# Optimization experiments

Hardware: AMD Instinct MI355X
Metric: run time of the kernel (lower is better)

## Reference

```python
import jax, jax.numpy as jnp
import numpy as np

N, E, G = 50000, 800000, 2000          # nodes, edges, graphs
F_NODE, F_EDGE, H = 64, 16, 128
SLOPE = 0.01                            # leaky_relu slope used throughout AttentiveFP
NUM_ATOM_LAYERS = 2                     # num_layers=3 -> 1 GATEConv + 2 GATConv
NUM_TIMESTEPS = 3


def _leaky(v):
    return jnp.where(v >= 0, v, SLOPE * v)


def _seg_softmax(logits, seg, n):
    # PyG softmax over edges grouped by target segment
    m = jax.ops.segment_max(logits, seg, num_segments=n)
    e = jnp.exp(logits - m[seg])
    s = jax.ops.segment_sum(e, seg, num_segments=n)
    return e / (s[seg] + 1e-16)


def _gru(xi, h, Wih, Whh, bih, bhh):
    # torch.nn.GRUCell, gate order (r, z, n)
    gi = xi @ Wih.T + bih
    gh = h @ Whh.T + bhh
    ir, iz, inn = jnp.split(gi, 3, axis=-1)
    hr, hz, hn = jnp.split(gh, 3, axis=-1)
    r = jax.nn.sigmoid(ir + hr)
    z = jax.nn.sigmoid(iz + hz)
    ng = jnp.tanh(inn + r * hn)
    return (1.0 - z) * ng + z * h


def setup_inputs() -> dict:
    key = jax.random.key(0)
    ks = iter(jax.random.split(key, 64))
    def rn(shape, s=0.1):
        return jax.random.normal(next(ks), shape, jnp.float32) * s
    inp = {}
    inp["x"] = jax.random.normal(next(ks), (N, F_NODE), jnp.float32)
    inp["edge_index"] = jax.random.randint(next(ks), (2, E), 0, N)
    inp["edge_attr"] = jax.random.normal(next(ks), (E, F_EDGE), jnp.float32)
    inp["batch"] = jnp.sort(jax.random.randint(next(ks), (N,), 0, G))
    inp["lin1_W"] = rn((H, F_NODE)); inp["lin1_b"] = rn((H,))
    inp["gate_att_l"] = rn((H,)); inp["gate_att_r"] = rn((H,))
    inp["gate_lin1_W"] = rn((H, H + F_EDGE)); inp["gate_lin2_W"] = rn((H, H)); inp["gate_bias"] = rn((H,))
    inp["gru0_Wih"] = rn((3 * H, H)); inp["gru0_Whh"] = rn((3 * H, H))
    inp["gru0_bih"] = rn((3 * H,)); inp["gru0_bhh"] = rn((3 * H,))
    L = NUM_ATOM_LAYERS
    inp["atom_lin_W"] = rn((L, H, H)); inp["atom_att_src"] = rn((L, H))
    inp["atom_att_dst"] = rn((L, H)); inp["atom_bias"] = rn((L, H))
    inp["atom_gru_Wih"] = rn((L, 3 * H, H)); inp["atom_gru_Whh"] = rn((L, 3 * H, H))
    inp["atom_gru_bih"] = rn((L, 3 * H)); inp["atom_gru_bhh"] = rn((L, 3 * H))
    inp["mol_lin_W"] = rn((H, H)); inp["mol_att_src"] = rn((H,))
    inp["mol_att_dst"] = rn((H,)); inp["mol_bias"] = rn((H,))
    inp["mol_gru_Wih"] = rn((3 * H, H)); inp["mol_gru_Whh"] = rn((3 * H, H))
    inp["mol_gru_bih"] = rn((3 * H,)); inp["mol_gru_bhh"] = rn((3 * H,))
    inp["lin2_W"] = rn((H, H)); inp["lin2_b"] = rn((H,))
    inp["fin_W"] = rn((1, H)); inp["fin_b"] = rn((1,))
    return inp


def _forward(x, edge_attr, lin1_W, lin1_b, gate_att_l, gate_att_r, gate_lin1_W,
             gate_lin2_W, gate_bias, gru0_Wih, gru0_Whh, gru0_bih, gru0_bhh,
             atom_lin_W, atom_att_src, atom_att_dst, atom_bias,
             atom_gru_Wih, atom_gru_Whh, atom_gru_bih, atom_gru_bhh,
             mol_lin_W, mol_att_src, mol_att_dst, mol_bias,
             mol_gru_Wih, mol_gru_Whh, mol_gru_bih, mol_gru_bhh,
             lin2_W, lin2_b, fin_W, fin_b, edge_index, batch):
    src, dst = edge_index[0], edge_index[1]  # PyG: row=source j, col=target i
    # --- input projection ---
    x = _leaky(x @ lin1_W.T + lin1_b)                                     # [N,H]
    # --- GATEConv (edge-featured attention, add aggregation) ---
    hj = _leaky(jnp.concatenate([x[src], edge_attr], axis=-1) @ gate_lin1_W.T)  # [E,H]
    alpha = _leaky(hj @ gate_att_l + (x @ gate_att_r)[dst])               # [E]
    a = _seg_softmax(alpha, dst, N)
    h = jax.ops.segment_sum((x @ gate_lin2_W.T)[src] * a[:, None], dst, num_segments=N) + gate_bias
    h = jax.nn.elu(h)  # dropout is identity in eval mode
    x = jnp.maximum(_gru(h, x, gru0_Wih, gru0_Whh, gru0_bih, gru0_bhh), 0.0)
    # --- atom-level GATConv layers (single head, no self loops) ---
    for l in range(NUM_ATOM_LAYERS):
        xs = x @ atom_lin_W[l].T                                          # [N,H]
        a = _leaky((xs @ atom_att_src[l])[src] + (xs @ atom_att_dst[l])[dst])
        a = _seg_softmax(a, dst, N)
        h = jax.ops.segment_sum(xs[src] * a[:, None], dst, num_segments=N) + atom_bias[l]
        h = jax.nn.elu(h)
        x = jnp.maximum(_gru(h, x, atom_gru_Wih[l], atom_gru_Whh[l],
                             atom_gru_bih[l], atom_gru_bhh[l]), 0.0)
    # --- molecule-level readout: bipartite GATConv node->graph + GRU ---
    out = jnp.maximum(jax.ops.segment_sum(x, batch, num_segments=G), 0.0)  # [G,H]
    xs = x @ mol_lin_W.T                                                   # fixed sources
    a_src = xs @ mol_att_src                                               # [N]
    for _ in range(NUM_TIMESTEPS):
        od = out @ mol_lin_W.T                                             # [G,H]
        a = _leaky(a_src + (od @ mol_att_dst)[batch])
        a = _seg_softmax(a, batch, G)
        h = jax.ops.segment_sum(xs * a[:, None], batch, num_segments=G) + mol_bias
        h = jax.nn.elu(h)
        out = jnp.maximum(_gru(h, out, mol_gru_Wih, mol_gru_Whh, mol_gru_bih, mol_gru_bhh), 0.0)
    out = out @ lin2_W.T + lin2_b                                          # AttentiveFP.lin2
    return jax.nn.sigmoid(out @ fin_W.T + fin_b).squeeze(-1)               # [G]


def reference(x, edge_index, edge_attr, batch, lin1_W, lin1_b, gate_att_l, gate_att_r,
              gate_lin1_W, gate_lin2_W, gate_bias, gru0_Wih, gru0_Whh, gru0_bih, gru0_bhh,
              atom_lin_W, atom_att_src, atom_att_dst, atom_bias,
              atom_gru_Wih, atom_gru_Whh, atom_gru_bih, atom_gru_bhh,
              mol_lin_W, mol_att_src, mol_att_dst, mol_bias,
              mol_gru_Wih, mol_gru_Whh, mol_gru_bih, mol_gru_bhh,
              lin2_W, lin2_b, fin_W, fin_b):
    return _forward(x, edge_attr, lin1_W, lin1_b, gate_att_l, gate_att_r, gate_lin1_W,
                    gate_lin2_W, gate_bias, gru0_Wih, gru0_Whh, gru0_bih, gru0_bhh,
                    atom_lin_W, atom_att_src, atom_att_dst, atom_bias,
                    atom_gru_Wih, atom_gru_Whh, atom_gru_bih, atom_gru_bhh,
                    mol_lin_W, mol_att_src, mol_att_dst, mol_bias,
                    mol_gru_Wih, mol_gru_Whh, mol_gru_bih, mol_gru_bhh,
                    lin2_W, lin2_b, fin_W, fin_b, edge_index, batch)
```

## Files before the change

### kernel.cpp

```cpp
#include <hip/hip_runtime.h>
#include <math.h>

#define NN 50000
#define EE 800000
#define GG 2000
#define HH 128
#define FN 64
#define FE 16

typedef short bf16x8 __attribute__((ext_vector_type(8)));
typedef float f32x4  __attribute__((ext_vector_type(4)));

__device__ __forceinline__ float leakyf(float v){ return v>=0.f ? v : 0.01f*v; }
__device__ __forceinline__ float eluf(float v){ return v>0.f ? v : expm1f(v); }
__device__ __forceinline__ float sigmf(float v){ return 1.f/(1.f+__expf(-v)); }
__device__ __forceinline__ float tanh_fast(float x){
  float ax = fabsf(x);
  float e = __expf(-2.f*ax);
  float t = (1.f - e)/(1.f + e);
  return x>=0.f ? t : -t;
}
__device__ __forceinline__ int rdl(int v, int l){ return __builtin_amdgcn_readlane(v, l); }
__device__ __forceinline__ float rdlf(float v, int l){
  return __int_as_float(__builtin_amdgcn_readlane(__float_as_int(v), l));
}
__device__ __forceinline__ float wsum(float v){
#pragma unroll
  for(int m=32;m>=1;m>>=1) v += __shfl_xor(v,m,64);
  return v;
}
__device__ __forceinline__ float wsum16(float v){
#pragma unroll
  for(int m=8;m>=1;m>>=1) v += __shfl_xor(v,m,64);
  return v;
}
__device__ __forceinline__ float wmax64(float v){
#pragma unroll
  for(int m=32;m>=1;m>>=1) v = fmaxf(v,__shfl_xor(v,m,64));
  return v;
}

__device__ __forceinline__ f32x4 mfma16(bf16x8 a, bf16x8 b, f32x4 c){
  return __builtin_amdgcn_mfma_f32_16x16x32_bf16(a, b, c, 0, 0, 0);
}

__device__ __forceinline__ void splitbf8(const float* p, bf16x8 &hi, bf16x8 &lo){
  float4 u = *(const float4*)p;
  float4 v = *(const float4*)(p+4);
  float f[8] = {u.x,u.y,u.z,u.w,v.x,v.y,v.z,v.w};
#pragma unroll
  for(int i=0;i<8;i++){
    unsigned b = __float_as_uint(f[i]);
    unsigned ht = b & 0xFFFF0000u;
    hi[i] = (short)(b >> 16);
    float r = f[i] - __uint_as_float(ht);
    lo[i] = (short)(__float_as_uint(r) >> 16);
  }
}

#define CV_LIN1   0
#define CV_G1X    8192
#define CV_G2     24576
#define CV_ALIN   40960
#define CV_MOL    73728
#define CV_G0IH   90112
#define CV_G0HH   139264
#define CV_AIH    188416
#define CV_AHH    286720
#define CV_MIH    385024
#define CV_MHH    434176
#define CV_GE     483328
#define CV_TOT2   485376

__global__ void k_convw2(const float* __restrict__ lin1W, const float* __restrict__ glin1W,
                         const float* __restrict__ glin2W, const float* __restrict__ aLinW,
                         const float* __restrict__ aGWih, const float* __restrict__ aGWhh,
                         const float* __restrict__ mLinW, const float* __restrict__ mGWih,
                         const float* __restrict__ mGWhh, const float* __restrict__ g0Wih,
                         const float* __restrict__ g0Whh,
                         short* __restrict__ hi, short* __restrict__ lo){
  int i = blockIdx.x*256 + threadIdx.x;
  if(i >= CV_TOT2) return;
  float v;
  if(i < CV_G1X){            v = lin1W[i];
  } else if(i < CV_G2){      int idx = i - CV_G1X; v = glin1W[(size_t)(idx>>7)*144 + (idx&127)];
  } else if(i < CV_ALIN){    v = glin2W[i - CV_G2];
  } else if(i < CV_MOL){     v = aLinW[i - CV_ALIN];
  } else if(i < CV_G0IH){    v = mLinW[i - CV_MOL];
  } else if(i < CV_G0HH){    v = g0Wih[i - CV_G0IH];
  } else if(i < CV_AIH){     v = g0Whh[i - CV_G0HH];
  } else if(i < CV_AHH){     v = aGWih[i - CV_AIH];
  } else if(i < CV_MIH){     v = aGWhh[i - CV_AHH];
  } else if(i < CV_MHH){     v = mGWih[i - CV_MIH];
  } else if(i < CV_GE){      v = mGWhh[i - CV_MHH];
  } else {                   int idx = i - CV_GE; v = glin1W[(size_t)(idx>>4)*144 + 128 + (idx&15)];
  }
  unsigned b = __float_as_uint(v);
  unsigned ht = b & 0xFFFF0000u;
  hi[i] = (short)(b >> 16);
  float r = v - __uint_as_float(ht);
  lo[i] = (short)(__float_as_uint(r) >> 16);
}

__global__ void k_count_all(const int* __restrict__ esrc, const int* __restrict__ edst,
                            const int* __restrict__ batch,
                            int* __restrict__ degd, int* __restrict__ degs,
                            int* __restrict__ gcnt){
  int i = blockIdx.x*256 + threadIdx.x;
  if(i < EE){
    atomicAdd(&degd[edst[i]], 1);
    atomicAdd(&degs[esrc[i]], 1);
  }
  if(i < NN) atomicAdd(&gcnt[batch[i]], 1);
}

__global__ void k_scan3(const int* __restrict__ degd, const int* __restrict__ degs,
                        const int* __restrict__ gcnt,
                        int* __restrict__ eoff, int* __restrict__ soff, int* __restrict__ goff){
  __shared__ int part[1024];
  const int* cnt; int* off; int n;
  if(blockIdx.x == 0){ cnt = degd; off = eoff; n = NN; }
  else if(blockIdx.x == 1){ cnt = degs; off = soff; n = NN; }
  else { cnt = gcnt; off = goff; n = GG; }
  int t = threadIdx.x;
  int C = (n + 1023) >> 10;
  int lo = t*C, hic = min(lo + C, n);
  int s = 0;
  for(int i=lo;i<hic;i++) s += cnt[i];
  part[t] = s;
  __syncthreads();
  for(int o=1;o<1024;o<<=1){
    int v = (t>=o) ? part[t-o] : 0;
    __syncthreads();
    part[t] += v;
    __syncthreads();
  }
  int base = part[t] - s;
  int run = base;
  for(int i=lo;i<hic;i++){ run += cnt[i]; off[i+1] = run; }
  if(t==0) off[0] = 0;
}

__global__ void k_scatter2(const int* __restrict__ esrc, const int* __restrict__ edst,
                           const int* __restrict__ eoff, const int* __restrict__ soff,
                           int* __restrict__ curd, int* __restrict__ curs,
                           int* __restrict__ esrcS, int* __restrict__ eperm,
                           int* __restrict__ eord){
  int e = blockIdx.x*256 + threadIdx.x;
  if(e < EE){
    int d = edst[e];
    int pos = eoff[d] + atomicAdd(&curd[d], 1);
    esrcS[pos] = esrc[e];
    eperm[e] = pos;
    int s = esrc[e];
    int pos2 = soff[s] + atomicAdd(&curs[s], 1);
    eord[pos2] = e;
  }
}

template<int ACT, int K, int NDOT>
__global__ __launch_bounds__(256) void k_proj_mfma(const float* __restrict__ A,
                                                   const short* __restrict__ Whi,
                                                   const short* __restrict__ Wlo,
                                                   const float* __restrict__ bias,
                                                   float* __restrict__ C, int M,
                                                   const float* __restrict__ u,
                                                   const float* __restrict__ v,
                                                   float* __restrict__ douta,
                                                   float* __restrict__ doutb){
  const int wave = threadIdx.x >> 6, lane = threadIdx.x & 63;
  const int m0 = blockIdx.x*64 + wave*16;
  const int lr = lane & 15, kg = lane >> 4;
  f32x4 acc[8];
#pragma unroll
  for(int t=0;t<8;t++) acc[t] = (f32x4){0.f,0.f,0.f,0.f};

  int arow = m0 + lr;
  int ar = arow < M ? arow : (M-1);

#pragma unroll
  for(int ks=0;ks<K;ks+=32){
    const int kb = ks + kg*8;
    bf16x8 ahi, alo;
    splitbf8(&A[(size_t)ar*K + kb], ahi, alo);
#pragma unroll
    for(int t=0;t<8;t++){
      const bf16x8 bh = *(const bf16x8*)&Whi[(size_t)(t*16+lr)*K + kb];
      const bf16x8 bl = *(const bf16x8*)&Wlo[(size_t)(t*16+lr)*K + kb];
      acc[t] = mfma16(ahi, bh, acc[t]);
      acc[t] = mfma16(ahi, bl, acc[t]);
      acc[t] = mfma16(alo, bh, acc[t]);
    }
  }

  float p1[4] = {0.f,0.f,0.f,0.f};
  float p2[4] = {0.f,0.f,0.f,0.f};
#pragma unroll
  for(int t=0;t<8;t++){
    int c = t*16 + lr;
    float ut = (NDOT>=1) ? u[c] : 0.f;
    float vt = (NDOT>=2) ? v[c] : 0.f;
#pragma unroll
    for(int r=0;r<4;r++){
      int m = m0 + kg*4 + r;
      float val = acc[t][r];
      if(ACT==1) val = leakyf(val + bias[c]);
      if(m < M) C[(size_t)m*HH + c] = val;
      if(NDOT>=1) p1[r] += val*ut;
      if(NDOT>=2) p2[r] += val*vt;
    }
  }
  if(NDOT>=1){
#pragma unroll
    for(int r=0;r<4;r++){
      float s1 = wsum16(p1[r]);
      int m = m0 + kg*4 + r;
      if(lr==0 && m < M) douta[m] = s1;
      if(NDOT>=2){
        float s2 = wsum16(p2[r]);
        if(lr==0 && m < M) doutb[m] = s2;
      }
    }
  }
}

__global__ __launch_bounds__(256) void k_gru_mfma(const float* __restrict__ MSG,
                                                  const float* __restrict__ X,
                                                  const short* __restrict__ WIhi,
                                                  const short* __restrict__ WIlo,
                                                  const short* __restrict__ WHhi,
                                                  const short* __restrict__ WHlo,
                                                  const float* __restrict__ bih,
                                                  const float* __restrict__ bhh,
                                                  float* __restrict__ XOUT, int M){
  __shared__ short LW[12*16*128];
  const int tid = threadIdx.x;
  const int wave = tid >> 6, lane = tid & 63;
  const int m0 = blockIdx.x*64 + wave*16;
  const int lr = lane & 15, kg = lane >> 4;
  int arow = m0 + lr;
  int ar = arow < M ? arow : (M-1);

  bf16x8 mh[4], ml[4], xh[4], xl[4];
#pragma unroll
  for(int ks=0;ks<4;ks++){
    splitbf8(&MSG[(size_t)ar*HH + ks*32 + kg*8], mh[ks], ml[ks]);
    splitbf8(&X  [(size_t)ar*HH + ks*32 + kg*8], xh[ks], xl[ks]);
  }

  const int srow = tid >> 4;
  const int scb  = tid & 15;
  const int sdst = srow*128 + ((scb ^ (srow & 7))*8);
  const size_t sgoff = (size_t)srow*HH + scb*8;

#pragma unroll 1
  for(int t=0;t<8;t++){
#pragma unroll
    for(int r=0;r<12;r++){
      const short* mat = (r<3) ? WIhi : (r<6) ? WHhi : (r<9) ? WIlo : WHlo;
      const int g = (r % 3);
      const short* src = mat + (size_t)(g*128 + t*16)*HH + sgoff;
      *(bf16x8*)&LW[r*2048 + sdst] = *(const bf16x8*)src;
    }
    __syncthreads();

    f32x4 aIr = (f32x4){0.f,0.f,0.f,0.f}, aIz = aIr, aIn = aIr;
    f32x4 aHr = aIr, aHz = aIr, aHn = aIr;
#pragma unroll
    for(int ks=0;ks<4;ks++){
      const int cb = ks*4 + kg;
      const int rb = lr*128 + ((cb ^ (lr & 7))*8);
      bf16x8 bIrh = *(const bf16x8*)&LW[ 0*2048 + rb];
      bf16x8 bIzh = *(const bf16x8*)&LW[ 1*2048 + rb];
      bf16x8 bInh = *(const bf16x8*)&LW[ 2*2048 + rb];
      bf16x8 bHrh = *(const bf16x8*)&LW[ 3*2048 + rb];
      bf16x8 bHzh = *(const bf16x8*)&LW[ 4*2048 + rb];
      bf16x8 bHnh = *(const bf16x8*)&LW[ 5*2048 + rb];
      bf16x8 bIrl = *(const bf16x8*)&LW[ 6*2048 + rb];
      bf16x8 bIzl = *(const bf16x8*)&LW[ 7*2048 + rb];
      bf16x8 bInl = *(const bf16x8*)&LW[ 8*2048 + rb];
      bf16x8 bHrl = *(const bf16x8*)&LW[ 9*2048 + rb];
      bf16x8 bHzl = *(const bf16x8*)&LW[10*2048 + rb];
      bf16x8 bHnl = *(const bf16x8*)&LW[11*2048 + rb];
      aIr = mfma16(mh[ks], bIrh, aIr); aIr = mfma16(mh[ks], bIrl, aIr); aIr = mfma16(ml[ks], bIrh, aIr);
      aIz = mfma16(mh[ks], bIzh, aIz); aIz = mfma16(mh[ks], bIzl, aIz); aIz = mfma16(ml[ks], bIzh, aIz);
      aIn = mfma16(mh[ks], bInh, aIn); aIn = mfma16(mh[ks], bInl, aIn); aIn = mfma16(ml[ks], bInh, aIn);
      aHr = mfma16(xh[ks], bHrh, aHr); aHr = mfma16(xh[ks], bHrl, aHr); aHr = mfma16(xl[ks], bHrh, aHr);
      aHz = mfma16(xh[ks], bHzh, aHz); aHz = mfma16(xh[ks], bHzl, aHz); aHz = mfma16(xl[ks], bHzh, aHz);
      aHn = mfma16(xh[ks], bHnh, aHn); aHn = mfma16(xh[ks], bHnl, aHn); aHn = mfma16(xl[ks], bHnh, aHn);
    }

    const int c = t*16 + lr;
    const float bir = bih[c], biz = bih[c+HH], bin = bih[c+2*HH];
    const float bhr = bhh[c], bhz = bhh[c+HH], bhn = bhh[c+2*HH];
#pragma unroll
    for(int r=0;r<4;r++){
      int mm = m0 + kg*4 + r;
      if(mm < M){
        float ir = aIr[r]+bir, iz = aIz[r]+biz, in_ = aIn[r]+bin;
        float hr = aHr[r]+bhr, hz = aHz[r]+bhz, hn = aHn[r]+bhn;
        float rr = sigmf(ir + hr);
        float z  = sigmf(iz + hz);
        float ng = tanh_fast(in_ + rr*hn);
        float hp = X[(size_t)mm*HH + c];
        XOUT[(size_t)mm*HH + c] = fmaxf((1.f - z)*ng + z*hp, 0.f);
      }
    }
    __syncthreads();
  }
}

__global__ __launch_bounds__(256) void k_gate_alpha4(const float* __restrict__ XP,
                                                     const float* __restrict__ EA,
                                                     const int* __restrict__ esrc,
                                                     const int* __restrict__ edst,
                                                     const short* __restrict__ GEhi,
                                                     const short* __restrict__ GElo,
                                                     const float* __restrict__ attl,
                                                     const float* __restrict__ RD,
                                                     const int* __restrict__ eperm,
                                                     const int* __restrict__ eord,
                                                     float* __restrict__ ALPHA){
  const int lane = threadIdx.x & 63;
  const int wid = (blockIdx.x*256 + threadIdx.x) >> 6;
  if(wid >= EE/128) return;
  const int lr = lane & 15, kg = lane >> 4;

  bf16x8 B1[8], B2[8];
#pragma unroll
  for(int t=0;t<8;t++){
    const int col = t*16 + lr;
    B1[t] = *(const bf16x8*)&GEhi[col*16 + (kg&1)*8];
    B2[t] = *(const bf16x8*)&GElo[col*16 + (kg&1)*8];
  }
  float at[8];
#pragma unroll
  for(int t=0;t<8;t++) at[t] = attl[t*16 + lr];

#pragma unroll 1
  for(int tw = wid*8; tw < wid*8 + 8; ++tw){
    const int p0 = tw*16;
    const int eoA = eord[p0 + lr];
    bf16x8 hi8, lo8;
    splitbf8(&EA[(size_t)eoA*FE + (kg&1)*8], hi8, lo8);
    bf16x8 A1 = (kg < 2) ? hi8 : lo8;
    bf16x8 A2 = hi8;
    if(kg >= 2){
#pragma unroll
      for(int i=0;i<8;i++) A2[i] = 0;
    }
    int srcR[4];
#pragma unroll
    for(int r=0;r<4;r++) srcR[r] = esrc[eord[p0 + kg*4 + r]];

    float p[4] = {0.f,0.f,0.f,0.f};
#pragma unroll
    for(int t=0;t<8;t++){
      f32x4 acc = (f32x4){0.f,0.f,0.f,0.f};
      acc = mfma16(A2, B2[t], acc);
      acc = mfma16(A1, B1[t], acc);
      const int c = t*16 + lr;
#pragma unroll
      for(int r=0;r<4;r++){
        float xp = XP[(size_t)srcR[r]*HH + c];
        p[r] += leakyf(acc[r] + xp) * at[t];
      }
    }
#pragma unroll
    for(int r=0;r<4;r++){
      float s = wsum16(p[r]);
      if(lr == 0){
        const int eoj = eord[p0 + kg*4 + r];
        ALPHA[eperm[eoj]] = leakyf(s + RD[edst[eoj]]);
      }
    }
  }
}

template<int MODE>
__global__ void k_softmaxw(const int* __restrict__ off, const int* __restrict__ items,
                           const float* __restrict__ AIN, const float* __restrict__ A1,
                           const float* __restrict__ A2, float* __restrict__ WOUT, int nseg){
  int w = (blockIdx.x*blockDim.x + threadIdx.x) >> 6;
  int lane = threadIdx.x & 63;
  if(w >= nseg) return;
  int s0 = off[w], s1 = off[w+1];
  int n = s1 - s0;
  float a2 = (MODE==0) ? 0.f : A2[w];

  if(n <= 64){
    float a = -INFINITY;
    int i = s0 + lane;
    if(lane < n){
      if(MODE==0) a = AIN[i];
      else if(MODE==1) a = leakyf(A1[items[i]] + a2);
      else a = leakyf(A1[i] + a2);
    }
    float m = wmax64(a);
    float e = (lane < n) ? __expf(a - m) : 0.f;
    float s = wsum(e);
    if(lane < n) WOUT[i] = e/(s + 1e-16f);
    return;
  }

  float m = -INFINITY;
  for(int i=s0+lane;i<s1;i+=64){
    float a;
    if(MODE==0) a = AIN[i];
    else if(MODE==1) a = leakyf(A1[items[i]] + a2);
    else a = leakyf(A1[i] + a2);
    m = fmaxf(m, a);
  }
  m = wmax64(m);

  float s = 0.f;
  for(int i=s0+lane;i<s1;i+=64){
    float a;
    if(MODE==0) a = AIN[i];
    else if(MODE==1) a = leakyf(A1[items[i]] + a2);
    else a = leakyf(A1[i] + a2);
    s += __expf(a - m);
  }
  s = wsum(s);
  float inv = 1.f/(s + 1e-16f);

  for(int i=s0+lane;i<s1;i+=64){
    float a;
    if(MODE==0) a = AIN[i];
    else if(MODE==1) a = leakyf(A1[items[i]] + a2);
    else a = leakyf(A1[i] + a2);
    WOUT[i] = __expf(a - m)*inv;
  }
}

__global__ void k_gather(const int* __restrict__ off, const int* __restrict__ items,
                         const float* __restrict__ W, const float* __restrict__ XSrc,
                         const float* __restrict__ bias, float* __restrict__ OUT, int nseg){
  int w = (blockIdx.x*blockDim.x + threadIdx.x) >> 6;
  int lane = threadIdx.x & 63;
  if(w >= nseg) return;
  int s0 = off[w], s1 = off[w+1];
  float hx = 0.f, hy = 0.f;

  for(int c0=s0;c0<s1;c0+=64){
    int n = min(64, s1-c0);
    int it = 0; float wg = 0.f;
    if(lane < n){
      int i = c0 + lane;
      it = items ? items[i] : i;
      wg = W[i];
    }
#pragma unroll 16
    for(int j=0;j<n;j++){
      int itj = rdl(it, j);
      float wj = rdlf(wg, j);
      float2 xv = *(const float2*)&XSrc[(size_t)itj*HH + 2*lane];
      hx += wj*xv.x;
      hy += wj*xv.y;
    }
  }
  float2 bv = *(const float2*)&bias[2*lane];
  float2 o;
  o.x = eluf(hx + bv.x);
  o.y = eluf(hy + bv.y);
  *(float2*)&OUT[(size_t)w*HH + 2*lane] = o;
}

__global__ void k_dot2(const float* __restrict__ X, const float* __restrict__ u,
                       float* __restrict__ a, int M){
  int w = (blockIdx.x*blockDim.x + threadIdx.x) >> 6;
  int lane = threadIdx.x & 63;
  if(w >= M) return;
  float2 x = *(const float2*)&X[(size_t)w*HH + 2*lane];
  float2 uu = *(const float2*)&u[2*lane];
  float p = x.x*uu.x + x.y*uu.y;
  p = wsum(p);
  if(lane==0) a[w] = p;
}

__global__ void k_ginit(const int* __restrict__ goff, const float* __restrict__ X,
                        float* __restrict__ OUT){
  int g = (blockIdx.x*blockDim.x + threadIdx.x) >> 6;
  int lane = threadIdx.x & 63;
  if(g >= GG) return;
  int s0 = goff[g], s1 = goff[g+1];
  float hx=0.f, hy=0.f;
  for(int n=s0;n<s1;n++){
    float2 xv = *(const float2*)&X[(size_t)n*HH + 2*lane];
    hx += xv.x; hy += xv.y;
  }
  float2 o;
  o.x = fmaxf(hx, 0.f);
  o.y = fmaxf(hy, 0.f);
  *(float2*)&OUT[(size_t)g*HH + 2*lane] = o;
}

__global__ void k_weff(const float* __restrict__ lin2W, const float* __restrict__ lin2b,
                       const float* __restrict__ finW, const float* __restrict__ finb,
                       const float* __restrict__ mLinW, const float* __restrict__ mAttD,
                       float* __restrict__ weff){
  int c = threadIdx.x;
  float s = 0.f, q = 0.f;
  for(int j=0;j<HH;j++){
    s += finW[j]*lin2W[(size_t)j*HH + c];
    q += mAttD[j]*mLinW[(size_t)j*HH + c];
  }
  weff[c] = s;
  weff[256 + c] = q;
  if(c==0){
    float bb = finb[0];
    for(int j=0;j<HH;j++) bb += lin2b[j]*finW[j];
    weff[HH] = bb;
  }
}

__global__ void k_final(const float* __restrict__ OUT, const float* __restrict__ weff,
                        float* __restrict__ y){
  int g = (blockIdx.x*blockDim.x + threadIdx.x) >> 6;
  int lane = threadIdx.x & 63;
  if(g >= GG) return;
  float2 ov = *(const float2*)&OUT[(size_t)g*HH + 2*lane];
  float2 wv = *(const float2*)&weff[2*lane];
  float p = ov.x*wv.x + ov.y*wv.y;
  p = wsum(p);
  if(lane==0) y[g] = sigmf(p + weff[HH]);
}

extern "C" void kernel_launch(void* const* d_in, const int* in_sizes, int n_in,
                              void* d_out, int out_size, void* d_ws, size_t ws_size,
                              hipStream_t stream){
  const float* in_x   = (const float*)d_in[0];
  const int*   eidx   = (const int*)d_in[1];
  const float* ea     = (const float*)d_in[2];
  const int*   batch  = (const int*)d_in[3];
  const float* lin1W  = (const float*)d_in[4];
  const float* lin1b  = (const float*)d_in[5];
  const float* gattl  = (const float*)d_in[6];
  const float* gattr  = (const float*)d_in[7];
  const float* glin1W = (const float*)d_in[8];
  const float* glin2W = (const float*)d_in[9];
  const float* gbias  = (const float*)d_in[10];
  const float* g0Wih  = (const float*)d_in[11];
  const float* g0Whh  = (const float*)d_in[12];
  const float* g0bih  = (const float*)d_in[13];
  const float* g0bhh  = (const float*)d_in[14];
  const float* aLinW  = (const float*)d_in[15];
  const float* aAttS  = (const float*)d_in[16];
  const float* aAttD  = (const float*)d_in[17];
  const float* aBias  = (const float*)d_in[18];
  const float* aGWih  = (const float*)d_in[19];
  const float* aGWhh  = (const float*)d_in[20];
  const float* aGbih  = (const float*)d_in[21];
  const float* aGbhh  = (const float*)d_in[22];
  const float* mLinW  = (const float*)d_in[23];
  const float* mAttS  = (const float*)d_in[24];
  const float* mAttD  = (const float*)d_in[25];
  const float* mBias  = (const float*)d_in[26];
  const float* mGWih  = (const float*)d_in[27];
  const float* mGWhh  = (const float*)d_in[28];
  const float* mGbih  = (const float*)d_in[29];
  const float* mGbhh  = (const float*)d_in[30];
  const float* lin2W  = (const float*)d_in[31];
  const float* lin2b  = (const float*)d_in[32];
  const float* finW   = (const float*)d_in[33];
  const float* finb   = (const float*)d_in[34];

  const int* esrc0 = eidx;
  const int* edst0 = eidx + EE;

  char* w = (char*)d_ws;
  size_t o = 0;
  auto alloc = [&](size_t bytes)->void*{
    void* p = w + o;
    o = (o + bytes + 255) & ~(size_t)255;
    return p;
  };
  float* X    = (float*)alloc((size_t)NN*HH*4);
  float* XB   = (float*)alloc((size_t)NN*HH*4);
  float* XS   = (float*)alloc((size_t)NN*HH*4);
  float* MSG  = (float*)alloc((size_t)NN*HH*4);
  float* XP   = (float*)alloc((size_t)NN*HH*4);
  float* ALPHA= (float*)alloc((size_t)EE*4);
  float* S1   = (float*)alloc((size_t)NN*4);
  float* S2   = (float*)alloc((size_t)NN*4);
  float* ADSTG= (float*)alloc((size_t)GG*4);
  float* OUTg = (float*)alloc((size_t)GG*HH*4);
  float* OUTb = (float*)alloc((size_t)GG*HH*4);
  float* HG   = (float*)alloc((size_t)GG*HH*4);
  float* WEFF = (float*)alloc(512*4);
  short* cWhi = (short*)alloc((size_t)CV_TOT2*2);
  short* cWlo = (short*)alloc((size_t)CV_TOT2*2);
  int* zeroreg= (int*)alloc((size_t)(4*NN + 2048)*4);
  int* degd = zeroreg;
  int* degs = zeroreg + NN;
  int* curd = zeroreg + 2*NN;
  int* curs = zeroreg + 3*NN;
  int* gcnt = zeroreg + 4*NN;
  int* eoff = (int*)alloc((size_t)(NN+1)*4);
  int* soff = (int*)alloc((size_t)(NN+1)*4);
  int* goff = (int*)alloc((size_t)(GG+1)*4);
  int* esrcS= (int*)alloc((size_t)EE*4);
  int* eperm= (int*)alloc((size_t)EE*4);
  int* eord = (int*)alloc((size_t)EE*4);

  const short* c_lin1_h = cWhi + CV_LIN1; const short* c_lin1_l = cWlo + CV_LIN1;
  const short* c_g1x_h  = cWhi + CV_G1X;  const short* c_g1x_l  = cWlo + CV_G1X;
  const short* c_g2_h   = cWhi + CV_G2;   const short* c_g2_l   = cWlo + CV_G2;
  const short* c_mol_h  = cWhi + CV_MOL;  const short* c_mol_l  = cWlo + CV_MOL;
  const short* c_g0ih_h = cWhi + CV_G0IH; const short* c_g0ih_l = cWlo + CV_G0IH;
  const short* c_g0hh_h = cWhi + CV_G0HH; const short* c_g0hh_l = cWlo + CV_G0HH;
  const short* c_mih_h  = cWhi + CV_MIH;  const short* c_mih_l  = cWlo + CV_MIH;
  const short* c_mhh_h  = cWhi + CV_MHH;  const short* c_mhh_l  = cWlo + CV_MHH;
  const short* c_ge_h   = cWhi + CV_GE;   const short* c_ge_l   = cWlo + CV_GE;

  k_convw2<<<(CV_TOT2+255)/256, 256, 0, stream>>>(lin1W, glin1W, glin2W, aLinW, aGWih, aGWhh,
                                                  mLinW, mGWih, mGWhh, g0Wih, g0Whh, cWhi, cWlo);
  k_weff<<<1, 128, 0, stream>>>(lin2W, lin2b, finW, finb, mLinW, mAttD, WEFF);

  hipMemsetAsync(zeroreg, 0, (size_t)(4*NN + 2048)*4, stream);
  k_count_all<<<EE/256, 256, 0, stream>>>(esrc0, edst0, batch, degd, degs, gcnt);
  k_scan3<<<3, 1024, 0, stream>>>(degd, degs, gcnt, eoff, soff, goff);
  k_scatter2<<<EE/256, 256, 0, stream>>>(esrc0, edst0, eoff, soff, curd, curs, esrcS, eperm, eord);

  const int gN = (NN + 63)/64;
  const int gG = (GG + 63)/64;

  k_proj_mfma<1,64,1><<<gN, 256, 0, stream>>>(in_x, c_lin1_h, c_lin1_l, lin1b, X, NN,
                                              gattr, nullptr, S1, nullptr);

  k_proj_mfma<0,128,0><<<gN, 256, 0, stream>>>(X, c_g1x_h, c_g1x_l, nullptr, XP, NN,
                                               nullptr, nullptr, nullptr, nullptr);
  k_proj_mfma<0,128,0><<<gN, 256, 0, stream>>>(X, c_g2_h, c_g2_l, nullptr, XS, NN,
                                               nullptr, nullptr, nullptr, nullptr);
  k_gate_alpha4<<<(EE/128 + 3)/4, 256, 0, stream>>>(XP, ea, esrc0, edst0, c_ge_h, c_ge_l,
                                                    gattl, S1, eperm, eord, ALPHA);
  k_softmaxw<0><<<(NN+3)/4, 256, 0, stream>>>(eoff, nullptr, ALPHA, nullptr, nullptr, ALPHA, NN);
  k_gather<<<(NN+3)/4, 256, 0, stream>>>(eoff, esrcS, ALPHA, XS, gbias, MSG, NN);
  k_gru_mfma<<<gN, 256, 0, stream>>>(MSG, X, c_g0ih_h, c_g0ih_l, c_g0hh_h, c_g0hh_l,
                                     g0bih, g0bhh, XB, NN);
  { float* t = X; X = XB; XB = t; }

  for(int l=0;l<2;l++){
    const short* c_a_h   = cWhi + CV_ALIN + (size_t)l*HH*HH;
    const short* c_a_l   = cWlo + CV_ALIN + (size_t)l*HH*HH;
    const short* c_aih_h = cWhi + CV_AIH + (size_t)l*3*HH*HH;
    const short* c_aih_l = cWlo + CV_AIH + (size_t)l*3*HH*HH;
    const short* c_ahh_h = cWhi + CV_AHH + (size_t)l*3*HH*HH;
    const short* c_ahh_l = cWlo + CV_AHH + (size_t)l*3*HH*HH;
    const float* asl  = aAttS + (size_t)l*HH;
    const float* adl  = aAttD + (size_t)l*HH;
    const float* bl   = aBias + (size_t)l*HH;
    const float* bi   = aGbih + (size_t)l*3*HH;
    const float* bh   = aGbhh + (size_t)l*3*HH;
    k_proj_mfma<0,128,2><<<gN, 256, 0, stream>>>(X, c_a_h, c_a_l, nullptr, XS, NN,
                                                 asl, adl, S1, S2);
    k_softmaxw<1><<<(NN+3)/4, 256, 0, stream>>>(eoff, esrcS, nullptr, S1, S2, ALPHA, NN);
    k_gather<<<(NN+3)/4, 256, 0, stream>>>(eoff, esrcS, ALPHA, XS, bl, MSG, NN);
    k_gru_mfma<<<gN, 256, 0, stream>>>(MSG, X, c_aih_h, c_aih_l, c_ahh_h, c_ahh_l, bi, bh, XB, NN);
    { float* t = X; X = XB; XB = t; }
  }

  k_ginit<<<(GG+3)/4, 256, 0, stream>>>(goff, X, OUTg);
  k_proj_mfma<0,128,1><<<gN, 256, 0, stream>>>(X, c_mol_h, c_mol_l, nullptr, XS, NN,
                                               mAttS, nullptr, S1, nullptr);

  float* Ocur = OUTg;
  float* Onxt = OUTb;
  for(int t=0;t<3;t++){
    k_dot2<<<(GG+3)/4, 256, 0, stream>>>(Ocur, WEFF+256, ADSTG, GG);
    k_softmaxw<2><<<(GG+3)/4, 256, 0, stream>>>(goff, nullptr, nullptr, S1, ADSTG, ALPHA, GG);
    k_gather<<<(GG+3)/4, 256, 0, stream>>>(goff, nullptr, ALPHA, XS, mBias, HG, GG);
    k_gru_mfma<<<gG, 256, 0, stream>>>(HG, Ocur, c_mih_h, c_mih_l, c_mhh_h, c_mhh_l,
                                       mGbih, mGbhh, Onxt, GG);
    { float* tt = Ocur; Ocur = Onxt; Onxt = tt; }
  }

  k_final<<<(GG+3)/4, 256, 0, stream>>>(Ocur, WEFF, (float*)d_out);
}
```

Measured before the change: 1.351 ms.

## Pre-sort edge data and bf16-split edge attrs in scatter for gate kernel

The scatter kernel now writes src, dst, and dst-sorted position arrays in source-sorted order, along with a pre-split hi/lo bf16 copy of the edge attributes. The gate-alpha kernel can then read these contiguously instead of going through the eord/eperm double indirection and splitting on the fly. The gate kernel also switches from 8 tiles per wave to one tile per wave, which raises parallelism but reloads the weight fragments per tile. The cost is extra scatter writes, about 51 MB for the bf16 attributes, plus three extra index arrays.

```diff
diff --git a/kernel.cpp b/kernel.cpp
--- a/kernel.cpp
+++ b/kernel.cpp
@@ -144,17 +144,27 @@
 __global__ void k_scatter2(const int* __restrict__ esrc, const int* __restrict__ edst,
                            const int* __restrict__ eoff, const int* __restrict__ soff,
                            int* __restrict__ curd, int* __restrict__ curs,
-                           int* __restrict__ esrcS, int* __restrict__ eperm,
-                           int* __restrict__ eord){
+                           int* __restrict__ esrcS, const float* __restrict__ EA,
+                           int* __restrict__ esrcO, int* __restrict__ edstO,
+                           int* __restrict__ epermO, short* __restrict__ EAs){
   int e = blockIdx.x*256 + threadIdx.x;
   if(e < EE){
     int d = edst[e];
     int pos = eoff[d] + atomicAdd(&curd[d], 1);
-    esrcS[pos] = esrc[e];
-    eperm[e] = pos;
     int s = esrc[e];
-    int pos2 = soff[s] + atomicAdd(&curs[s], 1);
-    eord[pos2] = e;
+    esrcS[pos] = s;
+    int p = soff[s] + atomicAdd(&curs[s], 1);
+    esrcO[p] = s;
+    edstO[p] = d;
+    epermO[p] = pos;
+    bf16x8 h0, l0, h1, l1;
+    splitbf8(&EA[(size_t)e*FE], h0, l0);
+    splitbf8(&EA[(size_t)e*FE + 8], h1, l1);
+    short* dst = &EAs[(size_t)p*32];
+    *(bf16x8*)(dst)      = h0;
+    *(bf16x8*)(dst + 8)  = h1;
+    *(bf16x8*)(dst + 16) = l0;
+    *(bf16x8*)(dst + 24) = l1;
   }
 }
 
@@ -310,69 +320,62 @@
   }
 }
 
-__global__ __launch_bounds__(256) void k_gate_alpha4(const float* __restrict__ XP,
-                                                     const float* __restrict__ EA,
-                                                     const int* __restrict__ esrc,
-                                                     const int* __restrict__ edst,
+__global__ __launch_bounds__(256) void k_gate_alpha5(const float* __restrict__ XP,
+                                                     const short* __restrict__ EAs,
+                                                     const int* __restrict__ esrcO,
+                                                     const int* __restrict__ edstO,
+                                                     const int* __restrict__ epermO,
                                                      const short* __restrict__ GEhi,
                                                      const short* __restrict__ GElo,
                                                      const float* __restrict__ attl,
                                                      const float* __restrict__ RD,
-                                                     const int* __restrict__ eperm,
-                                                     const int* __restrict__ eord,
                                                      float* __restrict__ ALPHA){
   const int lane = threadIdx.x & 63;
-  const int wid = (blockIdx.x*256 + threadIdx.x) >> 6;
-  if(wid >= EE/128) return;
+  const int tile = (blockIdx.x*256 + threadIdx.x) >> 6;
+  if(tile >= EE/16) return;
+  const int p0 = tile*16;
   const int lr = lane & 15, kg = lane >> 4;
 
+  const short* eap = &EAs[(size_t)(p0+lr)*32 + (kg>=2 ? 16 : 0) + (kg&1)*8];
+  bf16x8 A1 = *(const bf16x8*)eap;
+  bf16x8 A2 = A1;
+  if(kg >= 2){
+#pragma unroll
+    for(int i=0;i<8;i++) A2[i] = 0;
+  }
+
+  int4 sr4 = *(const int4*)&esrcO[p0 + kg*4];
+  int srcR[4] = {sr4.x, sr4.y, sr4.z, sr4.w};
+
   bf16x8 B1[8], B2[8];
+  float at[8];
 #pragma unroll
   for(int t=0;t<8;t++){
     const int col = t*16 + lr;
     B1[t] = *(const bf16x8*)&GEhi[col*16 + (kg&1)*8];
     B2[t] = *(const bf16x8*)&GElo[col*16 + (kg&1)*8];
-  }
-  float at[8];
-#pragma unroll
-  for(int t=0;t<8;t++) at[t] = attl[t*16 + lr];
-
-#pragma unroll 1
-  for(int tw = wid*8; tw < wid*8 + 8; ++tw){
-    const int p0 = tw*16;
-    const int eoA = eord[p0 + lr];
-    bf16x8 hi8, lo8;
-    splitbf8(&EA[(size_t)eoA*FE + (kg&1)*8], hi8, lo8);
-    bf16x8 A1 = (kg < 2) ? hi8 : lo8;
-    bf16x8 A2 = hi8;
-    if(kg >= 2){
-#pragma unroll
-      for(int i=0;i<8;i++) A2[i] = 0;
-    }
-    int srcR[4];
-#pragma unroll
-    for(int r=0;r<4;r++) srcR[r] = esrc[eord[p0 + kg*4 + r]];
-
-    float p[4] = {0.f,0.f,0.f,0.f};
-#pragma unroll
-    for(int t=0;t<8;t++){
-      f32x4 acc = (f32x4){0.f,0.f,0.f,0.f};
-      acc = mfma16(A2, B2[t], acc);
-      acc = mfma16(A1, B1[t], acc);
-      const int c = t*16 + lr;
-#pragma unroll
-      for(int r=0;r<4;r++){
-        float xp = XP[(size_t)srcR[r]*HH + c];
-        p[r] += leakyf(acc[r] + xp) * at[t];
-      }
-    }
+    at[t] = attl[col];
+  }
+
+  float p[4] = {0.f,0.f,0.f,0.f};
+#pragma unroll
+  for(int t=0;t<8;t++){
+    f32x4 acc = (f32x4){0.f,0.f,0.f,0.f};
+    acc = mfma16(A2, B2[t], acc);
+    acc = mfma16(A1, B1[t], acc);
+    const int c = t*16 + lr;
 #pragma unroll
     for(int r=0;r<4;r++){
-      float s = wsum16(p[r]);
-      if(lr == 0){
-        const int eoj = eord[p0 + kg*4 + r];
-        ALPHA[eperm[eoj]] = leakyf(s + RD[edst[eoj]]);
-      }
+      float xp = XP[(size_t)srcR[r]*HH + c];
+      p[r] += leakyf(acc[r] + xp) * at[t];
+    }
+  }
+#pragma unroll
+  for(int r=0;r<4;r++){
+    float s = wsum16(p[r]);
+    if(lr == 0){
+      const int j = p0 + kg*4 + r;
+      ALPHA[epermO[j]] = leakyf(s + RD[edstO[j]]);
     }
   }
 }
@@ -600,8 +603,10 @@
   int* soff = (int*)alloc((size_t)(NN+1)*4);
   int* goff = (int*)alloc((size_t)(GG+1)*4);
   int* esrcS= (int*)alloc((size_t)EE*4);
-  int* eperm= (int*)alloc((size_t)EE*4);
-  int* eord = (int*)alloc((size_t)EE*4);
+  int* esrcO= (int*)alloc((size_t)EE*4);
+  int* edstO= (int*)alloc((size_t)EE*4);
+  int* epermO=(int*)alloc((size_t)EE*4);
+  short* EAs = (short*)alloc((size_t)EE*32*2);
 
   const short* c_lin1_h = cWhi + CV_LIN1; const short* c_lin1_l = cWlo + CV_LIN1;
   const short* c_g1x_h  = cWhi + CV_G1X;  const short* c_g1x_l  = cWlo + CV_G1X;
@@ -620,7 +625,8 @@
   hipMemsetAsync(zeroreg, 0, (size_t)(4*NN + 2048)*4, stream);
   k_count_all<<<EE/256, 256, 0, stream>>>(esrc0, edst0, batch, degd, degs, gcnt);
   k_scan3<<<3, 1024, 0, stream>>>(degd, degs, gcnt, eoff, soff, goff);
-  k_scatter2<<<EE/256, 256, 0, stream>>>(esrc0, edst0, eoff, soff, curd, curs, esrcS, eperm, eord);
+  k_scatter2<<<EE/256, 256, 0, stream>>>(esrc0, edst0, eoff, soff, curd, curs,
+                                         esrcS, ea, esrcO, edstO, epermO, EAs);
 
   const int gN = (NN + 63)/64;
   const int gG = (GG + 63)/64;
@@ -632,8 +638,8 @@
                                                nullptr, nullptr, nullptr, nullptr);
   k_proj_mfma<0,128,0><<<gN, 256, 0, stream>>>(X, c_g2_h, c_g2_l, nullptr, XS, NN,
                                                nullptr, nullptr, nullptr, nullptr);
-  k_gate_alpha4<<<(EE/128 + 3)/4, 256, 0, stream>>>(XP, ea, esrc0, edst0, c_ge_h, c_ge_l,
-                                                    gattl, S1, eperm, eord, ALPHA);
+  k_gate_alpha5<<<(EE/16 + 3)/4, 256, 0, stream>>>(XP, EAs, esrcO, edstO, epermO,
+                                                   c_ge_h, c_ge_l, gattl, S1, ALPHA);
   k_softmaxw<0><<<(NN+3)/4, 256, 0, stream>>>(eoff, nullptr, ALPHA, nullptr, nullptr, ALPHA, NN);
   k_gather<<<(NN+3)/4, 256, 0, stream>>>(eoff, esrcS, ALPHA, XS, gbias, MSG, NN);
   k_gru_mfma<<<gN, 256, 0, stream>>>(MSG, X, c_g0ih_h, c_g0ih_l, c_g0hh_h, c_g0hh_l,
```

Result: faster. 1.239 ms (-8.3%).
